# Optimization experiments

Measured on AMD Instinct MI355X. Metric: run time of the kernel, lower is better.

Reference implementation:

```python
import jax, jax.numpy as jnp
import numpy as np
import math

# ---- model dims (match init_kwargs) ----
D_MODEL = 1024
EXPAND = 2
HEADDIM = 64
D_STATE = 128
NGROUPS = 1
CHUNK = 64
A_FLOOR = 1e-4
D_INNER = EXPAND * D_MODEL            # 2048
NHEADS = D_INNER // HEADDIM           # 32
ROPE_DIM = D_STATE // 2               # rope_fraction=0.5 -> rotate half the state dims
NROPE = ROPE_DIM // 2                 # 32 rotation angles
D_IN_PROJ = D_INNER + 2 * D_STATE * NGROUPS + 3 * NHEADS + NROPE  # 2432
B, L = 2, 2048
EPS = 1e-5


def setup_inputs() -> dict:
    key = jax.random.key(0)
    ks = jax.random.split(key, 5)
    u = jax.random.normal(ks[0], (B, L, D_MODEL), dtype=jnp.float32)
    W_in = jax.random.normal(ks[1], (D_IN_PROJ, D_MODEL), dtype=jnp.float32) * 0.02
    W_out = jax.random.normal(ks[2], (D_MODEL, D_INNER), dtype=jnp.float32) * 0.02
    # dt_bias init as in the torch module
    dt_min, dt_max, dt_floor = 1e-3, 1e-1, 1e-4
    dt = jnp.exp(jax.random.uniform(ks[3], (NHEADS,)) * (math.log(dt_max) - math.log(dt_min)) + math.log(dt_min))
    dt = jnp.maximum(dt, dt_floor)
    dt_bias = dt + jnp.log(-jnp.expm1(-dt))
    B_bias = jnp.ones((NHEADS, D_STATE), dtype=jnp.float32)
    C_bias = jnp.ones((NHEADS, D_STATE), dtype=jnp.float32)
    Bnorm_w = jnp.ones((D_STATE,), dtype=jnp.float32)
    Cnorm_w = jnp.ones((D_STATE,), dtype=jnp.float32)
    D = jnp.ones((NHEADS,), dtype=jnp.float32)
    return {"u": u, "W_in": W_in, "dt_bias": dt_bias, "B_bias": B_bias, "C_bias": C_bias,
            "Bnorm_w": Bnorm_w, "Cnorm_w": Cnorm_w, "D": D, "W_out": W_out}


def _rmsnorm(v, w):
    return v * jax.lax.rsqrt(jnp.mean(v * v, axis=-1, keepdims=True) + EPS) * w


def _rope(v, cos, sin):
    # rotate first 2*NROPE dims of last axis (pairs (i, i+NROPE)); rest untouched
    x1 = v[..., :NROPE]
    x2 = v[..., NROPE:2 * NROPE]
    rest = v[..., 2 * NROPE:]
    return jnp.concatenate([x1 * cos - x2 * sin, x1 * sin + x2 * cos, rest], axis=-1)


def _forward(u, W_in, dt_bias, B_bias, C_bias, Bnorm_w, Cnorm_w, D, W_out):
    b, l, _ = u.shape
    proj = jnp.einsum('bld,ed->ble', u, W_in)
    idx = np.cumsum([D_INNER, D_STATE * NGROUPS, D_STATE * NGROUPS, NHEADS, NHEADS, NHEADS])[:-1].tolist()
    x, Braw, Craw, dd_dt, dd_A, trap_angles = jnp.split(proj, [D_INNER, D_INNER + D_STATE, D_INNER + 2 * D_STATE,
                                                                D_INNER + 2 * D_STATE + NHEADS,
                                                                D_INNER + 2 * D_STATE + 2 * NHEADS], axis=-1)
    trap = trap_angles[..., :NHEADS]
    angles = trap_angles[..., NHEADS:NHEADS + NROPE]
    x = x.reshape(b, l, NHEADS, HEADDIM)

    # discretization scalars per (b,l,h)
    A = -jax.nn.softplus(dd_A)
    A = jnp.minimum(A, -A_FLOOR)
    DT = jax.nn.softplus(dd_dt + dt_bias)
    la = A * DT                      # log of per-step decay (negative)
    a = jnp.exp(la)

    # RMSNorm on B/C (ngroups=1), broadcast to heads, add per-head bias
    Bn = _rmsnorm(Braw, Bnorm_w)[:, :, None, :] + B_bias   # (b,l,h,n)
    Cn = _rmsnorm(Craw, Cnorm_w)[:, :, None, :] + C_bias

    # inline RoPE: cumulative angle Theta_t = cumsum(angles_t * dt_t)
    theta = angles[:, :, None, :] * DT[..., None]           # (b,l,h,r)
    Theta = jnp.cumsum(theta, axis=1)
    cosT, sinT = jnp.cos(Theta), jnp.sin(Theta)
    Bn = _rope(Bn, cosT, sinT)
    Cn = _rope(Cn, cosT, sinT)

    # trapezoidal integration weights: dt*(lam*B_t x_t + (1-lam)*exp(A dt)*B_{t-1} x_{t-1})
    lam = jax.nn.sigmoid(trap)
    w1 = DT * lam                    # current-token weight  (b,l,h)
    w2 = DT * (1.0 - lam) * a        # previous-token weight (includes decay)
    Bp = jnp.pad(Bn, ((0, 0), (1, 0), (0, 0), (0, 0)))[:, :-1]
    xp = jnp.pad(x, ((0, 0), (1, 0), (0, 0), (0, 0)))[:, :-1]

    # ---- chunked selective scan ----
    nc = l // CHUNK
    ck = lambda t: t.reshape(b, nc, CHUNK, *t.shape[2:])
    xc, xpc, Bc, Bpc, Cc = ck(x), ck(xp), ck(Bn), ck(Bp), ck(Cn)
    lac, w1c, w2c = ck(la), ck(w1), ck(w2)
    Acum = jnp.cumsum(lac, axis=2)                           # (b,z,t,h)

    mask = jnp.tril(jnp.ones((CHUNK, CHUNK), dtype=u.dtype))
    decay = jnp.exp(Acum[:, :, :, None, :] - Acum[:, :, None, :, :]) * mask[None, None, :, :, None]  # (b,z,t,s,h)

    CB1 = jnp.einsum('bzthn,bzshn->bztsh', Cc, Bc)
    CB2 = jnp.einsum('bzthn,bzshn->bztsh', Cc, Bpc)
    M1 = decay * CB1 * w1c[:, :, None, :, :]
    M2 = decay * CB2 * w2c[:, :, None, :, :]
    Yintra = jnp.einsum('bztsh,bzshp->bzthp', M1, xc) + jnp.einsum('bztsh,bzshp->bzthp', M2, xpc)

    # contribution of each chunk to its end-of-chunk state
    r = jnp.exp(Acum[:, :, -1:, :] - Acum)                   # (b,z,t,h)
    U = (jnp.einsum('bzsh,bzshn,bzshp->bzhpn', r * w1c, Bc, xc)
         + jnp.einsum('bzsh,bzshn,bzshp->bzhpn', r * w2c, Bpc, xpc))
    cd = jnp.exp(Acum[:, :, -1, :])                          # whole-chunk decay (b,z,h)

    def step(h, inp):
        U_, c_ = inp
        return c_[..., None, None] * h + U_, h               # emit state at chunk start
    h0 = jnp.zeros((b, NHEADS, HEADDIM, D_STATE), dtype=u.dtype)
    _, states = jax.lax.scan(step, h0, (jnp.moveaxis(U, 1, 0), jnp.moveaxis(cd, 1, 0)))  # (z,b,h,p,n)

    Ystate = jnp.einsum('bzthn,bzth,zbhpn->bzthp', Cc, jnp.exp(Acum), states)
    y = (Yintra + Ystate).reshape(b, l, NHEADS, HEADDIM) + x * D[None, None, :, None]
    y = y.reshape(b, l, D_INNER)
    return jnp.einsum('bli,oi->blo', y, W_out)


def reference(u, W_in, dt_bias, B_bias, C_bias, Bnorm_w, Cnorm_w, D, W_out):
    return _forward(u, W_in, dt_bias, B_bias, C_bias, Bnorm_w, Cnorm_w, D, W_out)
```

## Files before the change

kernel.cpp:

```cpp
#include <hip/hip_runtime.h>
#include <hip/hip_bf16.h>
#include <math.h>

typedef unsigned short u16;
typedef __attribute__((ext_vector_type(8))) short s16x8;
typedef __attribute__((ext_vector_type(4))) float f32x4;

#define BB 2
#define LL 2048
#define DMODEL 1024
#define DI 2048
#define NH 32
#define HD 64
#define DS 128
#define NR 32
#define CH 64
#define NC 32
#define DIP 2432
#define NTOK (BB*LL)
#define PAW 384
#define CVW 264

__device__ __forceinline__ float bf2f(u16 u){ union{unsigned i; float f;} c; c.i=((unsigned)u)<<16; return c.f; }
__device__ __forceinline__ u16 f2bf(float f){ __hip_bfloat16 h=__float2bfloat16(f); return *reinterpret_cast<u16*>(&h); }
__device__ __forceinline__ float softplusf(float x){ return fmaxf(x,0.f) + log1pf(expf(-fabsf(x))); }

__device__ __forceinline__ void gl_lds16(const void* g, void* l){
  __builtin_amdgcn_global_load_lds((const __attribute__((address_space(1))) void*)g,
                                   (__attribute__((address_space(3))) void*)l, 16, 0, 0);
}

__device__ __forceinline__ s16x8 ldswz(const u16* base, int r, int kunit){
  return *(const s16x8*)&base[r*128 + ((kunit ^ (r&7))<<3)];
}
__device__ __forceinline__ s16x8 ldswz64(const u16* base, int r, int kunit){
  return *(const s16x8*)&base[r*64 + ((kunit ^ (r&7))<<3)];
}
__device__ __forceinline__ float ldswz64_s(const u16* base, int r, int n){
  return bf2f(base[r*64 + (((n>>3) ^ (r&7))<<3) + (n&7)]);
}
__device__ __forceinline__ s16x8 ld72(const u16* base, int r, int kelem){
  return *(const s16x8*)&base[r*72 + kelem];
}

__global__ __launch_bounds__(256) void k_cast(const float* __restrict__ in, u16* __restrict__ out, int n){
  int i = (blockIdx.x*256 + threadIdx.x)*4;
  if (i < n){
    float4 v = *(const float4*)&in[i];
    ushort4 o; o.x=f2bf(v.x); o.y=f2bf(v.y); o.z=f2bf(v.z); o.w=f2bf(v.w);
    *(ushort4*)&out[i] = o;
  }
}

__global__ __launch_bounds__(512) void k_gemm_in(const u16* __restrict__ A,
                                                 const u16* __restrict__ Bm,
                                                 float* __restrict__ pAux,
                                                 u16* __restrict__ Xtg){
  __shared__ u16 lA[128*64];
  __shared__ u16 lB[128*64];
  int tid = threadIdx.x;
  int l = tid & 63, w = tid >> 6;
  int nwg = gridDim.x*gridDim.y;
  int flat = blockIdx.y*gridDim.x + blockIdx.x;
  int cpx = nwg >> 3;
  int swz = (flat & 7)*cpx + (flat >> 3);
  int bx = swz % gridDim.x, by = swz / gridDim.x;
  int bm = by*128, bn = bx*128;
  int wr = w >> 2, wc = w & 3;
  const f32x4 vzero = {0.f,0.f,0.f,0.f};
  f32x4 acc[4][2];
  #pragma unroll
  for (int i=0;i<4;i++)
    #pragma unroll
    for (int j=0;j<2;j++) acc[i][j] = vzero;

  for (int kt=0; kt<DMODEL; kt+=64){
    __syncthreads();
    #pragma unroll
    for (int cc=0; cc<2; cc++){
      int s = w*2 + cc;
      int uu = s*64 + l;
      int r = uu >> 3, jl = uu & 7;
      int j = jl ^ (r & 7);
      gl_lds16(A  + (size_t)(bm+r)*DMODEL + kt + j*8, &lA[s*512]);
      gl_lds16(Bm + (size_t)(bn+r)*DMODEL + kt + j*8, &lB[s*512]);
    }
    __syncthreads();
    #pragma unroll
    for (int ks=0; ks<2; ks++){
      s16x8 af[4], bf[2];
      #pragma unroll
      for (int i=0;i<4;i++){
        int row = wr*64 + i*16 + (l&15);
        int j = ks*4 + (l>>4);
        af[i] = *(const s16x8*)&lA[row*64 + (j^(row&7))*8];
      }
      #pragma unroll
      for (int i=0;i<2;i++){
        int row = wc*32 + i*16 + (l&15);
        int j = ks*4 + (l>>4);
        bf[i] = *(const s16x8*)&lB[row*64 + (j^(row&7))*8];
      }
      #pragma unroll
      for (int i=0;i<4;i++)
        #pragma unroll
        for (int jj=0;jj<2;jj++)
          acc[i][jj] = __builtin_amdgcn_mfma_f32_16x16x32_bf16(af[i], bf[jj], acc[i][jj], 0,0,0);
    }
  }
  int col0 = bn + wc*32 + (l&15);
  int row0 = bm + wr*64 + (l>>4)*4;
  if (bn < DI){
    int h = (bn + wc*32) >> 6;
    int pbase = (wc & 1)*32 + (l&15);
    int b = bm >> 11;
    #pragma unroll
    for (int i=0;i<4;i++){
      int lbase = (bm & (LL-1)) + wr*64 + (l>>4)*4 + i*16;
      #pragma unroll
      for (int jj=0;jj<2;jj++){
        int p = pbase + jj*16;
        ushort4 o;
        o.x = f2bf(acc[i][jj][0]); o.y = f2bf(acc[i][jj][1]);
        o.z = f2bf(acc[i][jj][2]); o.w = f2bf(acc[i][jj][3]);
        *(ushort4*)&Xtg[((size_t)(b*NH + h)*HD + p)*LL + lbase] = o;
      }
    }
  } else {
    #pragma unroll
    for (int i=0;i<4;i++)
      #pragma unroll
      for (int jj=0;jj<2;jj++)
        #pragma unroll
        for (int q=0;q<4;q++)
          pAux[(size_t)(row0 + i*16 + q)*PAW + col0 + jj*16 - DI] = acc[i][jj][q];
  }
}

__global__ __launch_bounds__(256) void k_prep(const float* __restrict__ pAux,
                                              const float* __restrict__ dt_bias,
                                              const float* __restrict__ Bnw,
                                              const float* __restrict__ Cnw,
                                              float* __restrict__ Bnr, float* __restrict__ Cnr,
                                              float* __restrict__ DTg, float* __restrict__ lag,
                                              float* __restrict__ w1g, float* __restrict__ w2g){
  int tid = threadIdx.x;
  int r = tid >> 7, t = tid & 127;
  int row = blockIdx.x*2 + r;
  const float* pr = pAux + (size_t)row*PAW;
  float bv = pr[t], cv = pr[128+t];
  float sb = bv*bv, sc = cv*cv;
  for (int o=32;o;o>>=1){ sb += __shfl_down(sb,o); sc += __shfl_down(sc,o); }
  __shared__ float red[8];
  if ((tid&63)==0){ red[(tid>>6)*2]=sb; red[(tid>>6)*2+1]=sc; }
  __syncthreads();
  float ssb = red[r*4]+red[r*4+2], ssc = red[r*4+1]+red[r*4+3];
  float rb = rsqrtf(ssb/DS + 1e-5f), rc = rsqrtf(ssc/DS + 1e-5f);
  Bnr[(size_t)row*DS+t] = bv*rb*Bnw[t];
  Cnr[(size_t)row*DS+t] = cv*rc*Cnw[t];
  if (t < NH){
    int h = t;
    float Av = -softplusf(pr[288+h]); Av = fminf(Av, -1e-4f);
    float DT = softplusf(pr[256+h] + dt_bias[h]);
    float la = Av*DT;
    float lam = 1.f/(1.f+expf(-pr[320+h]));
    DTg[row*NH+h] = DT;
    lag[row*NH+h] = la;
    w1g[row*NH+h] = DT*lam;
    w2g[row*NH+h] = DT*(1.f-lam)*expf(la);
  }
}

__global__ __launch_bounds__(64) void k_theta_part(const float* __restrict__ pAux, const float* __restrict__ DTg,
                                                   float* __restrict__ Spart){
  int blk = blockIdx.x*2 + (threadIdx.x>>5);
  int j = threadIdx.x & 31;
  int h = blk % NH; int z = (blk/NH)%NC; int b = blk/(NH*NC);
  float acc = 0.f;
  for (int i=0;i<CH;i++){
    int row = b*LL + z*CH + i;
    acc += DTg[row*NH+h] * pAux[(size_t)row*PAW + 352 + j];
  }
  Spart[(size_t)blk*NR + j] = acc;
}

__global__ void k_theta_scan(float* __restrict__ Spart){
  int idx = blockIdx.x*blockDim.x + threadIdx.x;
  int j = idx % NR; int h = (idx/NR)%NH; int b = idx/(NR*NH);
  float acc = 0.f;
  for (int z=0;z<NC;z++){
    size_t o = (size_t)((b*NC+z)*NH + h)*NR + j;
    float t = Spart[o]; Spart[o] = acc; acc += t;
  }
}

__global__ __launch_bounds__(64) void k_theta_full(const float* __restrict__ pAux, const float* __restrict__ DTg,
                                                   const float* __restrict__ Spart, float* __restrict__ Theta){
  int blk = blockIdx.x*2 + (threadIdx.x>>5);
  int j = threadIdx.x & 31;
  int h = blk % NH; int z = (blk/NH)%NC; int b = blk/(NH*NC);
  float acc = Spart[(size_t)blk*NR + j];
  for (int i=0;i<CH;i++){
    int row = b*LL + z*CH + i;
    acc += DTg[row*NH+h] * pAux[(size_t)row*PAW + 352 + j];
    Theta[((size_t)row*NH + h)*NR + j] = acc;
  }
}

__global__ __launch_bounds__(256) void k_acum(const float* __restrict__ lag,
                                              const float* __restrict__ w1g,
                                              const float* __restrict__ w2g,
                                              float* __restrict__ CV,
                                              float* __restrict__ Acumg,
                                              float* __restrict__ cdg){
  int blk = blockIdx.x*4 + (threadIdx.x>>6);
  int l = threadIdx.x & 63;
  int h = blk & 31, z = (blk>>5)&31, b = blk>>10;
  int row = b*LL + z*CH + l;
  float la = lag[row*NH+h], w1 = w1g[row*NH+h], w2 = w2g[row*NH+h];
  float a = la;
  #pragma unroll
  for (int o=1;o<64;o<<=1){ float t = __shfl_up(a,o); a += (l>=o) ? t : 0.f; }
  float Acm = __shfl(a, 31);
  float Alast = __shfl(a, 63);
  float eA = expf(a - Acm);
  float emA = expf(Acm - a);
  float rfac = expf(Alast - a);
  float rw1 = rfac*w1, rw2 = rfac*w2;
  float rw1p = __shfl_up(rw1, 1);
  float* cv = CV + (size_t)blk*CVW;
  cv[l] = eA;
  cv[64 + l] = emA*w1;
  cv[128 + l] = emA*w2;
  cv[192 + l] = (l>0 ? rw1p : 0.f) + rw2;
  if (l == 63){ cv[192+64] = rw1; cdg[blk] = expf(Alast); }
  Acumg[(size_t)blk*CH + l] = a;
}

__global__ __launch_bounds__(256) void k_rope2(const float* __restrict__ Bnr,
                                               const float* __restrict__ Cnr,
                                               const float* __restrict__ Theta,
                                               const float* __restrict__ B_bias,
                                               const float* __restrict__ C_bias,
                                               const float* __restrict__ CV,
                                               u16* __restrict__ Bn, u16* __restrict__ Cn,
                                               u16* __restrict__ BTw){
  __shared__ float vwS[65];
  __shared__ u16 BTt[128][68];
  int blk = blockIdx.x; int h = blk&31, z=(blk>>5)&31, b=blk>>10;
  int l0 = z*CH; int tid = threadIdx.x;
  if (tid < 65) vwS[tid] = CV[(size_t)blk*CVW + 192 + tid];
  __syncthreads();
  #pragma unroll
  for (int it=0; it<8; it++){
    int idx = it*256 + tid;
    int r = idx>>5, j = idx&31;
    int row = b*LL + l0 + r;
    const float* br = Bnr + (size_t)row*DS;
    const float* cr = Cnr + (size_t)row*DS;
    const float* bb = B_bias + h*DS;
    const float* cb = C_bias + h*DS;
    float th = Theta[((size_t)row*NH + h)*NR + j];
    float cs = cosf(th), sn = sinf(th);
    float b0 = br[j]    + bb[j];
    float b1 = br[j+32] + bb[j+32];
    float b2 = br[j+64] + bb[j+64];
    float b3 = br[j+96] + bb[j+96];
    float c0 = cr[j]    + cb[j];
    float c1 = cr[j+32] + cb[j+32];
    float c2 = cr[j+64] + cb[j+64];
    float c3 = cr[j+96] + cb[j+96];
    float obA = b0*cs - b1*sn, obB = b0*sn + b1*cs;
    float ocA = c0*cs - c1*sn, ocB = c0*sn + c1*cs;
    u16* bnp = Bn + ((size_t)row*NH + h)*DS;
    u16* cnp = Cn + ((size_t)row*NH + h)*DS;
    bnp[j]    = f2bf(obA); bnp[j+32] = f2bf(obB);
    bnp[j+64] = f2bf(b2);  bnp[j+96] = f2bf(b3);
    cnp[j]    = f2bf(ocA); cnp[j+32] = f2bf(ocB);
    cnp[j+64] = f2bf(c2);  cnp[j+96] = f2bf(c3);
    float vwr = vwS[r+1];
    BTt[j][r]    = f2bf(obA*vwr);
    BTt[j+32][r] = f2bf(obB*vwr);
    BTt[j+64][r] = f2bf(b2*vwr);
    BTt[j+96][r] = f2bf(b3*vwr);
  }
  __syncthreads();
  for (int it=0; it<8; it++){
    int idx = it*256 + tid;
    int n = idx>>4, rg = (idx&15)*4;
    ushort4 o4 = *(ushort4*)&BTt[n][rg];
    *(ushort4*)&BTw[((size_t)((b*NH+h)*DS) + n)*LL + l0 + rg] = o4;
  }
}

__global__ __launch_bounds__(256) void k_chunk_a(
    const u16* __restrict__ Xtg, const u16* __restrict__ Bn,
    const u16* __restrict__ Cn, const u16* __restrict__ BTw,
    const float* __restrict__ CV, const float* __restrict__ Dgl,
    u16* __restrict__ Yb, u16* __restrict__ Ugb){
  __shared__ u16 BsBT[65*128];
  __shared__ u16 CsMc[64*128];
  __shared__ u16 Xt64[64*64];
  __shared__ u16 Bp[128], Xp[64];
  __shared__ float cvS[260];
  __shared__ float mc0s[64];
  int blk = blockIdx.x;
  int h = blk&31, z=(blk>>5)&31, b=blk>>10;
  int l0 = z*CH;
  int tid = threadIdx.x; int l = tid&63, w = tid>>6;
  size_t bh = (size_t)(b*NH + h);

  if (tid < 128){
    u16 v = 0;
    if (z > 0) v = Bn[((size_t)(b*LL+l0-1)*NH + h)*DS + tid];
    BsBT[tid] = v; Bp[tid] = v;
  } else if (tid < 192){
    int p = tid - 128;
    u16 v = 0;
    if (z > 0) v = Xtg[(bh*HD + p)*LL + l0 - 1];
    Xp[p] = v;
  }
  cvS[tid] = CV[(size_t)blk*CVW + tid];
  if (tid == 0) cvS[256] = CV[(size_t)blk*CVW + 256];
  #pragma unroll
  for (int cc=0; cc<4; cc++){
    int c = w*4 + cc;
    { int r = 1 + 4*c + (l>>4);
      gl_lds16(Bn + ((size_t)(b*LL+l0+r-1)*NH+h)*DS + (((l&15)^(r&7))<<3), &BsBT[(1+4*c)*128]); }
    { int r = 4*c + (l>>4);
      gl_lds16(Cn + ((size_t)(b*LL+l0+r)*NH+h)*DS + (((l&15)^(r&7))<<3), &CsMc[4*c*128]); }
  }
  #pragma unroll
  for (int cc=0; cc<2; cc++){
    int s = w*2 + cc;
    int uu = s*64 + l; int r = uu>>3, jl = uu&7, j = jl^(r&7);
    gl_lds16(Xtg + (bh*HD + r)*LL + l0 + j*8, &Xt64[s*512]);
  }
  __syncthreads();

  const f32x4 vzero = {0.f,0.f,0.f,0.f};
  f32x4 acb[4];
  #pragma unroll
  for (int j=0;j<4;j++) acb[j] = vzero;
  #pragma unroll
  for (int ks=0; ks<4; ks++){
    s16x8 af = ldswz(CsMc, 16*w + (l&15), ks*4 + (l>>4));
    #pragma unroll
    for (int j=0;j<4;j++){
      s16x8 bfr = ldswz(BsBT, 1 + 16*j + (l&15), ks*4 + (l>>4));
      acb[j] = __builtin_amdgcn_mfma_f32_16x16x32_bf16(af, bfr, acb[j], 0,0,0);
    }
  }
  {
    int t = tid>>2, part = tid&3;
    float s = 0.f;
    #pragma unroll
    for (int uu=0; uu<4; uu++){
      int u = part*4 + uu;
      s16x8 cr = *(const s16x8*)&CsMc[t*128 + ((u^(t&7))<<3)];
      s16x8 br = *(const s16x8*)&BsBT[u<<3];
      #pragma unroll
      for (int e=0;e<8;e++) s += bf2f(cr[e])*bf2f(br[e]);
    }
    s += __shfl_xor(s, 1); s += __shfl_xor(s, 2);
    if (part == 0) mc0s[t] = s * cvS[t] * cvS[128];
  }
  __syncthreads();

  #pragma unroll
  for (int cc=0; cc<4; cc++){
    int c = w*4 + cc;
    int uu = c*64 + l; int r = uu>>3, jl = uu&7, j = jl^(r&7);
    gl_lds16(BTw + (bh*DS + r)*LL + l0 + j*8, &BsBT[c*512]);
  }
  #pragma unroll
  for (int j=0;j<4;j++){
    #pragma unroll
    for (int q=0;q<4;q++){
      int t = 16*w + (l>>4)*4 + q;
      int k = 16*j + (l&15);
      int sp = k + 1;
      float g = 0.f;
      if (sp <= t+1) g += cvS[63+sp];
      if (sp <= t)   g += cvS[128+sp];
      g *= cvS[t];
      CsMc[t*72 + k] = f2bf(acb[j][q] * g);
    }
  }
  __syncthreads();

  f32x4 ay[4];
  #pragma unroll
  for (int j=0;j<4;j++) ay[j] = vzero;
  #pragma unroll
  for (int ks=0; ks<2; ks++){
    s16x8 af = ld72(CsMc, 16*w + (l&15), ks*32 + (l>>4)*8);
    #pragma unroll
    for (int j=0;j<4;j++){
      s16x8 bfr = ldswz64(Xt64, 16*j + (l&15), ks*4 + (l>>4));
      ay[j] = __builtin_amdgcn_mfma_f32_16x16x32_bf16(af, bfr, ay[j], 0,0,0);
    }
  }
  {
    float Dh = Dgl[h];
    #pragma unroll
    for (int j=0;j<4;j++){
      #pragma unroll
      for (int q=0;q<4;q++){
        int t = 16*w + (l>>4)*4 + q;
        int p = 16*j + (l&15);
        float xval = ldswz64_s(Xt64, p, t);
        float yv = ay[j][q] + mc0s[t]*bf2f(Xp[p]) + Dh*xval;
        Yb[((size_t)(b*LL + l0 + t))*DI + h*HD + p] = f2bf(yv);
      }
    }
  }

  f32x4 au[8];
  #pragma unroll
  for (int j=0;j<8;j++) au[j] = vzero;
  #pragma unroll
  for (int ks=0; ks<2; ks++){
    s16x8 af = ldswz64(Xt64, 16*w + (l&15), ks*4 + (l>>4));
    #pragma unroll
    for (int j=0;j<8;j++){
      s16x8 bfr = ldswz64(BsBT, 16*j + (l&15), ks*4 + (l>>4));
      au[j] = __builtin_amdgcn_mfma_f32_16x16x32_bf16(af, bfr, au[j], 0,0,0);
    }
  }
  {
    float vw0 = cvS[192];
    #pragma unroll
    for (int j=0;j<8;j++){
      #pragma unroll
      for (int q=0;q<4;q++){
        int p = 16*w + (l>>4)*4 + q;
        int n = 16*j + (l&15);
        float uv = au[j][q] + vw0*bf2f(Xp[p])*bf2f(Bp[n]);
        Ugb[(size_t)blk*(HD*DS) + p*DS + n] = f2bf(uv);
      }
    }
  }
}

__global__ __launch_bounds__(256) void k_scan(u16* __restrict__ Ugb, const float* __restrict__ cdg){
  int idx = blockIdx.x*256 + threadIdx.x;
  int pn = idx % (HD*DS);
  int h  = (idx/(HD*DS)) % NH;
  int b  = idx/(HD*DS*NH);
  float hs = 0.f;
  for (int z=0;z<NC;z++){
    size_t o = ((size_t)((b*NC+z)*NH) + h)*(HD*DS) + pn;
    float tmp = bf2f(Ugb[o]);
    Ugb[o] = f2bf(hs);
    hs = cdg[(b*NC+z)*NH + h]*hs + tmp;
  }
}

__global__ __launch_bounds__(256) void k_state(
    const u16* __restrict__ Cn, const u16* __restrict__ Ugb,
    const float* __restrict__ Acumg, u16* __restrict__ Yb){
  __shared__ u16 Cs[64*128];
  __shared__ u16 Sb[64*128];
  __shared__ float eAs[64];
  int blk = blockIdx.x;
  int h = blk & 31, z = (blk>>5)&31, b = blk>>10;
  int l0 = z*CH;
  int tid = threadIdx.x;
  int l = tid & 63, w = tid >> 6;

  if (tid < 64) eAs[tid] = expf(Acumg[(size_t)blk*CH + tid]);
  #pragma unroll
  for (int cc=0; cc<4; cc++){
    int c = w*4 + cc;
    int r = 4*c + (l>>4);
    gl_lds16(Cn + ((size_t)(b*LL + l0 + r)*NH + h)*DS + (((l&15)^(r&7))<<3), &Cs[4*c*128]);
    gl_lds16(Ugb + (size_t)blk*(HD*DS) + (size_t)r*DS + (((l&15)^(r&7))<<3), &Sb[4*c*128]);
  }
  __syncthreads();

  f32x4 as[4];
  const f32x4 vzero = {0.f,0.f,0.f,0.f};
  #pragma unroll
  for (int j=0;j<4;j++) as[j] = vzero;
  #pragma unroll
  for (int ks=0; ks<4; ks++){
    s16x8 af = ldswz(Cs, 16*w + (l&15), ks*4 + (l>>4));
    #pragma unroll
    for (int j=0;j<4;j++){
      s16x8 bfr = ldswz(Sb, 16*j + (l&15), ks*4 + (l>>4));
      as[j] = __builtin_amdgcn_mfma_f32_16x16x32_bf16(af, bfr, as[j], 0,0,0);
    }
  }
  #pragma unroll
  for (int j=0;j<4;j++){
    #pragma unroll
    for (int q=0;q<4;q++){
      int t = 16*w + (l>>4)*4 + q;
      int p = 16*j + (l&15);
      size_t idx = ((size_t)(b*LL + l0 + t))*DI + h*HD + p;
      Yb[idx] = f2bf(bf2f(Yb[idx]) + eAs[t]*as[j][q]);
    }
  }
}

template<int N, int K>
__global__ __launch_bounds__(512) void k_mfma_nt(const u16* __restrict__ A,
                                                 const u16* __restrict__ Bm,
                                                 float* __restrict__ C){
  __shared__ u16 lA[128*64];
  __shared__ u16 lB[128*64];
  int tid = threadIdx.x;
  int l = tid & 63, w = tid >> 6;
  int nwg = gridDim.x*gridDim.y;
  int flat = blockIdx.y*gridDim.x + blockIdx.x;
  int cpx = nwg >> 3;
  int swz = (flat & 7)*cpx + (flat >> 3);
  int bx = swz % gridDim.x, by = swz / gridDim.x;
  int bm = by*128, bn = bx*128;
  int wr = w >> 2, wc = w & 3;
  const f32x4 vzero = {0.f,0.f,0.f,0.f};
  f32x4 acc[4][2];
  #pragma unroll
  for (int i=0;i<4;i++)
    #pragma unroll
    for (int j=0;j<2;j++) acc[i][j] = vzero;

  for (int kt=0; kt<K; kt+=64){
    __syncthreads();
    #pragma unroll
    for (int cc=0; cc<2; cc++){
      int s = w*2 + cc;
      int uu = s*64 + l;
      int r = uu >> 3, jl = uu & 7;
      int j = jl ^ (r & 7);
      gl_lds16(A  + (size_t)(bm+r)*K + kt + j*8, &lA[s*512]);
      gl_lds16(Bm + (size_t)(bn+r)*K + kt + j*8, &lB[s*512]);
    }
    __syncthreads();
    #pragma unroll
    for (int ks=0; ks<2; ks++){
      s16x8 af[4], bf[2];
      #pragma unroll
      for (int i=0;i<4;i++){
        int row = wr*64 + i*16 + (l&15);
        int j = ks*4 + (l>>4);
        af[i] = *(const s16x8*)&lA[row*64 + (j^(row&7))*8];
      }
      #pragma unroll
      for (int i=0;i<2;i++){
        int row = wc*32 + i*16 + (l&15);
        int j = ks*4 + (l>>4);
        bf[i] = *(const s16x8*)&lB[row*64 + (j^(row&7))*8];
      }
      #pragma unroll
      for (int i=0;i<4;i++)
        #pragma unroll
        for (int jj=0;jj<2;jj++)
          acc[i][jj] = __builtin_amdgcn_mfma_f32_16x16x32_bf16(af[i], bf[jj], acc[i][jj], 0,0,0);
    }
  }
  int col0 = bn + wc*32 + (l&15);
  int row0 = bm + wr*64 + (l>>4)*4;
  #pragma unroll
  for (int i=0;i<4;i++)
    #pragma unroll
    for (int jj=0;jj<2;jj++)
      #pragma unroll
      for (int q=0;q<4;q++)
        C[(size_t)(row0 + i*16 + q)*N + col0 + jj*16] = acc[i][jj][q];
}

constexpr size_t OFF_PAUX  = 0;
constexpr size_t OFF_XTG   = 6291456;
constexpr size_t OFF_BNR   = 23068672;
constexpr size_t OFF_CNR   = 25165824;
constexpr size_t OFF_DT    = 27262976;
constexpr size_t OFF_LA    = 27787264;
constexpr size_t OFF_W1    = 28311552;
constexpr size_t OFF_W2    = 28835840;
constexpr size_t OFF_SPART = 29360128;
constexpr size_t OFF_CV    = 29622272;
constexpr size_t OFF_ACUM  = 31784960;
constexpr size_t OFF_CD    = 32309248;
constexpr size_t OFF_THETA = 32317440;
constexpr size_t OFF_Y     = OFF_THETA;
constexpr size_t OFF_BN    = 49094656;
constexpr size_t OFF_CN    = 82649088;
constexpr size_t OFF_BTW   = 116203520;
constexpr size_t OFF_R1    = 149757952;
constexpr size_t OFF_UBF   = OFF_R1;
constexpr size_t OFF_WINBF = OFF_R1 + 16777216;
constexpr size_t OFF_UGB   = OFF_R1;
constexpr size_t OFF_WOUTBF= OFF_PAUX;

extern "C" void kernel_launch(void* const* d_in, const int* in_sizes, int n_in,
                              void* d_out, int out_size, void* d_ws, size_t ws_size,
                              hipStream_t stream) {
  const float* u       = (const float*)d_in[0];
  const float* W_in    = (const float*)d_in[1];
  const float* dt_bias = (const float*)d_in[2];
  const float* B_bias  = (const float*)d_in[3];
  const float* C_bias  = (const float*)d_in[4];
  const float* Bnw     = (const float*)d_in[5];
  const float* Cnw     = (const float*)d_in[6];
  const float* Dg      = (const float*)d_in[7];
  const float* W_out   = (const float*)d_in[8];
  float* out = (float*)d_out;
  char* ws = (char*)d_ws;

  float* pAux  = (float*)(ws + OFF_PAUX);
  u16*   Xtg   = (u16*)  (ws + OFF_XTG);
  float* Bnr   = (float*)(ws + OFF_BNR);
  float* Cnr   = (float*)(ws + OFF_CNR);
  float* DTg   = (float*)(ws + OFF_DT);
  float* lag   = (float*)(ws + OFF_LA);
  float* w1g   = (float*)(ws + OFF_W1);
  float* w2g   = (float*)(ws + OFF_W2);
  float* Spart = (float*)(ws + OFF_SPART);
  float* CVp   = (float*)(ws + OFF_CV);
  float* Acumg = (float*)(ws + OFF_ACUM);
  float* cdg   = (float*)(ws + OFF_CD);
  float* Theta = (float*)(ws + OFF_THETA);
  u16*   Yb    = (u16*)  (ws + OFF_Y);
  u16*   Bn    = (u16*)  (ws + OFF_BN);
  u16*   Cn    = (u16*)  (ws + OFF_CN);
  u16*   BTw   = (u16*)  (ws + OFF_BTW);
  u16*   u_bf  = (u16*)  (ws + OFF_UBF);
  u16*   Win_bf= (u16*)  (ws + OFF_WINBF);
  u16*   Ugb   = (u16*)  (ws + OFF_UGB);
  u16*   Wout_bf=(u16*)  (ws + OFF_WOUTBF);

  k_cast<<<(NTOK*DMODEL)/1024, 256, 0, stream>>>(u, u_bf, NTOK*DMODEL);
  k_cast<<<(DIP*DMODEL)/1024, 256, 0, stream>>>(W_in, Win_bf, DIP*DMODEL);
  k_gemm_in<<<dim3(DIP/128, NTOK/128), 512, 0, stream>>>(u_bf, Win_bf, pAux, Xtg);

  k_prep      <<<NTOK/2, 256, 0, stream>>>(pAux, dt_bias, Bnw, Cnw, Bnr, Cnr, DTg, lag, w1g, w2g);
  k_theta_part<<<(BB*NC*NH)/2, 64, 0, stream>>>(pAux, DTg, Spart);
  k_theta_scan<<<(BB*NH*NR)/256, 256, 0, stream>>>(Spart);
  k_theta_full<<<(BB*NC*NH)/2, 64, 0, stream>>>(pAux, DTg, Spart, Theta);
  k_acum      <<<(BB*NC*NH)/4, 256, 0, stream>>>(lag, w1g, w2g, CVp, Acumg, cdg);
  k_rope2     <<<BB*NC*NH, 256, 0, stream>>>(Bnr, Cnr, Theta, B_bias, C_bias, CVp, Bn, Cn, BTw);

  k_chunk_a<<<BB*NC*NH, 256, 0, stream>>>(Xtg, Bn, Cn, BTw, CVp, Dg, Yb, Ugb);
  k_scan   <<<(BB*NH*HD*DS)/256, 256, 0, stream>>>(Ugb, cdg);
  k_state  <<<BB*NC*NH, 256, 0, stream>>>(Cn, Ugb, Acumg, Yb);

  k_cast<<<(DMODEL*DI)/1024, 256, 0, stream>>>(W_out, Wout_bf, DMODEL*DI);
  k_mfma_nt<DMODEL, DI><<<dim3(DMODEL/128, NTOK/128), 512, 0, stream>>>(Yb, Wout_bf, out);

  (void)in_sizes; (void)n_in; (void)out_size; (void)ws_size;
}
```

Baseline: 189.7 us.

## Fuse B rope into chunk kernel and vectorize the inter-chunk scan

B-side RoPE, bias add and the weighted transposed copy are now computed inside k_chunk_a directly into shared memory, instead of being written to global Bn/BTw buffers and reloaded. This removes two large per-head bf16 intermediates and their global round trips. The Y buffer moves to a separate workspace offset, since it can no longer alias Theta, which k_chunk_a now reads. k_scan now handles 8 state elements per thread with 16-byte loads and stores, using fewer threads. The cost is extra trig and LDS work in the chunk kernel, plus less parallelism in the scan.

```diff
diff --git a/kernel.cpp b/kernel.cpp
--- a/kernel.cpp
+++ b/kernel.cpp
@@ -32,6 +32,9 @@
 
 __device__ __forceinline__ s16x8 ldswz(const u16* base, int r, int kunit){
   return *(const s16x8*)&base[r*128 + ((kunit ^ (r&7))<<3)];
+}
+__device__ __forceinline__ int swze(int row, int n){
+  return row*128 + ((((n>>3) ^ (row&7))<<3) | (n&7));
 }
 __device__ __forceinline__ s16x8 ldswz64(const u16* base, int r, int kunit){
   return *(const s16x8*)&base[r*64 + ((kunit ^ (r&7))<<3)];
@@ -237,69 +240,41 @@
   Acumg[(size_t)blk*CH + l] = a;
 }
 
-__global__ __launch_bounds__(256) void k_rope2(const float* __restrict__ Bnr,
-                                               const float* __restrict__ Cnr,
+__global__ __launch_bounds__(256) void k_ropeC(const float* __restrict__ Cnr,
                                                const float* __restrict__ Theta,
-                                               const float* __restrict__ B_bias,
                                                const float* __restrict__ C_bias,
-                                               const float* __restrict__ CV,
-                                               u16* __restrict__ Bn, u16* __restrict__ Cn,
-                                               u16* __restrict__ BTw){
-  __shared__ float vwS[65];
-  __shared__ u16 BTt[128][68];
+                                               u16* __restrict__ Cn){
   int blk = blockIdx.x; int h = blk&31, z=(blk>>5)&31, b=blk>>10;
   int l0 = z*CH; int tid = threadIdx.x;
-  if (tid < 65) vwS[tid] = CV[(size_t)blk*CVW + 192 + tid];
-  __syncthreads();
+  const float* cb = C_bias + h*DS;
   #pragma unroll
   for (int it=0; it<8; it++){
     int idx = it*256 + tid;
     int r = idx>>5, j = idx&31;
     int row = b*LL + l0 + r;
-    const float* br = Bnr + (size_t)row*DS;
     const float* cr = Cnr + (size_t)row*DS;
-    const float* bb = B_bias + h*DS;
-    const float* cb = C_bias + h*DS;
     float th = Theta[((size_t)row*NH + h)*NR + j];
     float cs = cosf(th), sn = sinf(th);
-    float b0 = br[j]    + bb[j];
-    float b1 = br[j+32] + bb[j+32];
-    float b2 = br[j+64] + bb[j+64];
-    float b3 = br[j+96] + bb[j+96];
     float c0 = cr[j]    + cb[j];
     float c1 = cr[j+32] + cb[j+32];
     float c2 = cr[j+64] + cb[j+64];
     float c3 = cr[j+96] + cb[j+96];
-    float obA = b0*cs - b1*sn, obB = b0*sn + b1*cs;
     float ocA = c0*cs - c1*sn, ocB = c0*sn + c1*cs;
-    u16* bnp = Bn + ((size_t)row*NH + h)*DS;
     u16* cnp = Cn + ((size_t)row*NH + h)*DS;
-    bnp[j]    = f2bf(obA); bnp[j+32] = f2bf(obB);
-    bnp[j+64] = f2bf(b2);  bnp[j+96] = f2bf(b3);
     cnp[j]    = f2bf(ocA); cnp[j+32] = f2bf(ocB);
     cnp[j+64] = f2bf(c2);  cnp[j+96] = f2bf(c3);
-    float vwr = vwS[r+1];
-    BTt[j][r]    = f2bf(obA*vwr);
-    BTt[j+32][r] = f2bf(obB*vwr);
-    BTt[j+64][r] = f2bf(b2*vwr);
-    BTt[j+96][r] = f2bf(b3*vwr);
-  }
-  __syncthreads();
-  for (int it=0; it<8; it++){
-    int idx = it*256 + tid;
-    int n = idx>>4, rg = (idx&15)*4;
-    ushort4 o4 = *(ushort4*)&BTt[n][rg];
-    *(ushort4*)&BTw[((size_t)((b*NH+h)*DS) + n)*LL + l0 + rg] = o4;
   }
 }
 
 __global__ __launch_bounds__(256) void k_chunk_a(
-    const u16* __restrict__ Xtg, const u16* __restrict__ Bn,
-    const u16* __restrict__ Cn, const u16* __restrict__ BTw,
+    const u16* __restrict__ Xtg, const float* __restrict__ Bnr,
+    const u16* __restrict__ Cn, const float* __restrict__ Theta,
+    const float* __restrict__ B_bias,
     const float* __restrict__ CV, const float* __restrict__ Dgl,
     u16* __restrict__ Yb, u16* __restrict__ Ugb){
-  __shared__ u16 BsBT[65*128];
+  __shared__ u16 Bs[65*128];
   __shared__ u16 CsMc[64*128];
+  __shared__ u16 Bt[128*72];
   __shared__ u16 Xt64[64*64];
   __shared__ u16 Bp[128], Xp[64];
   __shared__ float cvS[260];
@@ -310,25 +285,19 @@
   int tid = threadIdx.x; int l = tid&63, w = tid>>6;
   size_t bh = (size_t)(b*NH + h);
 
-  if (tid < 128){
-    u16 v = 0;
-    if (z > 0) v = Bn[((size_t)(b*LL+l0-1)*NH + h)*DS + tid];
-    BsBT[tid] = v; Bp[tid] = v;
-  } else if (tid < 192){
+  cvS[tid] = CV[(size_t)blk*CVW + tid];
+  if (tid == 0) cvS[256] = CV[(size_t)blk*CVW + 256];
+  if (tid >= 128 && tid < 192){
     int p = tid - 128;
     u16 v = 0;
     if (z > 0) v = Xtg[(bh*HD + p)*LL + l0 - 1];
     Xp[p] = v;
   }
-  cvS[tid] = CV[(size_t)blk*CVW + tid];
-  if (tid == 0) cvS[256] = CV[(size_t)blk*CVW + 256];
   #pragma unroll
   for (int cc=0; cc<4; cc++){
     int c = w*4 + cc;
-    { int r = 1 + 4*c + (l>>4);
-      gl_lds16(Bn + ((size_t)(b*LL+l0+r-1)*NH+h)*DS + (((l&15)^(r&7))<<3), &BsBT[(1+4*c)*128]); }
-    { int r = 4*c + (l>>4);
-      gl_lds16(Cn + ((size_t)(b*LL+l0+r)*NH+h)*DS + (((l&15)^(r&7))<<3), &CsMc[4*c*128]); }
+    int r = 4*c + (l>>4);
+    gl_lds16(Cn + ((size_t)(b*LL+l0+r)*NH+h)*DS + (((l&15)^(r&7))<<3), &CsMc[4*c*128]);
   }
   #pragma unroll
   for (int cc=0; cc<2; cc++){
@@ -338,6 +307,54 @@
   }
   __syncthreads();
 
+  {
+    const float* bb = B_bias + h*DS;
+    #pragma unroll
+    for (int it=0; it<8; it++){
+      int idx = it*256 + tid;
+      int r = idx>>5, j = idx&31;
+      int row = b*LL + l0 + r;
+      const float* br = Bnr + (size_t)row*DS;
+      float th = Theta[((size_t)row*NH + h)*NR + j];
+      float cs = cosf(th), sn = sinf(th);
+      float b0 = br[j]    + bb[j];
+      float b1 = br[j+32] + bb[j+32];
+      float b2 = br[j+64] + bb[j+64];
+      float b3 = br[j+96] + bb[j+96];
+      float obA = b0*cs - b1*sn, obB = b0*sn + b1*cs;
+      int rr = r + 1;
+      Bs[swze(rr, j)]    = f2bf(obA);
+      Bs[swze(rr, j+32)] = f2bf(obB);
+      Bs[swze(rr, j+64)] = f2bf(b2);
+      Bs[swze(rr, j+96)] = f2bf(b3);
+      float vwr = cvS[192 + rr];
+      Bt[j*72 + r]      = f2bf(obA*vwr);
+      Bt[(j+32)*72 + r] = f2bf(obB*vwr);
+      Bt[(j+64)*72 + r] = f2bf(b2*vwr);
+      Bt[(j+96)*72 + r] = f2bf(b3*vwr);
+    }
+    if (tid < 32){
+      int j = tid;
+      float obA=0.f, obB=0.f, b2=0.f, b3=0.f;
+      if (z > 0){
+        int row = b*LL + l0 - 1;
+        const float* br = Bnr + (size_t)row*DS;
+        float th = Theta[((size_t)row*NH + h)*NR + j];
+        float cs = cosf(th), sn = sinf(th);
+        float b0 = br[j]    + bb[j];
+        float b1 = br[j+32] + bb[j+32];
+        b2 = br[j+64] + bb[j+64];
+        b3 = br[j+96] + bb[j+96];
+        obA = b0*cs - b1*sn; obB = b0*sn + b1*cs;
+      }
+      Bs[j]    = f2bf(obA); Bs[j+32] = f2bf(obB);
+      Bs[j+64] = f2bf(b2);  Bs[j+96] = f2bf(b3);
+      Bp[j]    = f2bf(obA); Bp[j+32] = f2bf(obB);
+      Bp[j+64] = f2bf(b2);  Bp[j+96] = f2bf(b3);
+    }
+  }
+  __syncthreads();
+
   const f32x4 vzero = {0.f,0.f,0.f,0.f};
   f32x4 acb[4];
   #pragma unroll
@@ -347,7 +364,7 @@
     s16x8 af = ldswz(CsMc, 16*w + (l&15), ks*4 + (l>>4));
     #pragma unroll
     for (int j=0;j<4;j++){
-      s16x8 bfr = ldswz(BsBT, 1 + 16*j + (l&15), ks*4 + (l>>4));
+      s16x8 bfr = ldswz(Bs, 1 + 16*j + (l&15), ks*4 + (l>>4));
       acb[j] = __builtin_amdgcn_mfma_f32_16x16x32_bf16(af, bfr, acb[j], 0,0,0);
     }
   }
@@ -358,7 +375,7 @@
     for (int uu=0; uu<4; uu++){
       int u = part*4 + uu;
       s16x8 cr = *(const s16x8*)&CsMc[t*128 + ((u^(t&7))<<3)];
-      s16x8 br = *(const s16x8*)&BsBT[u<<3];
+      s16x8 br = *(const s16x8*)&Bs[u<<3];
       #pragma unroll
       for (int e=0;e<8;e++) s += bf2f(cr[e])*bf2f(br[e]);
     }
@@ -367,12 +384,6 @@
   }
   __syncthreads();
 
-  #pragma unroll
-  for (int cc=0; cc<4; cc++){
-    int c = w*4 + cc;
-    int uu = c*64 + l; int r = uu>>3, jl = uu&7, j = jl^(r&7);
-    gl_lds16(BTw + (bh*DS + r)*LL + l0 + j*8, &BsBT[c*512]);
-  }
   #pragma unroll
   for (int j=0;j<4;j++){
     #pragma unroll
@@ -424,7 +435,7 @@
     s16x8 af = ldswz64(Xt64, 16*w + (l&15), ks*4 + (l>>4));
     #pragma unroll
     for (int j=0;j<8;j++){
-      s16x8 bfr = ldswz64(BsBT, 16*j + (l&15), ks*4 + (l>>4));
+      s16x8 bfr = ld72(Bt, 16*j + (l&15), ks*32 + (l>>4)*8);
       au[j] = __builtin_amdgcn_mfma_f32_16x16x32_bf16(af, bfr, au[j], 0,0,0);
     }
   }
@@ -445,15 +456,24 @@
 
 __global__ __launch_bounds__(256) void k_scan(u16* __restrict__ Ugb, const float* __restrict__ cdg){
   int idx = blockIdx.x*256 + threadIdx.x;
-  int pn = idx % (HD*DS);
-  int h  = (idx/(HD*DS)) % NH;
-  int b  = idx/(HD*DS*NH);
-  float hs = 0.f;
+  int pn8 = (idx & 1023)*8;
+  int h  = (idx >> 10) & 31;
+  int b  = idx >> 15;
+  float hs[8];
+  #pragma unroll
+  for (int e=0;e<8;e++) hs[e] = 0.f;
   for (int z=0;z<NC;z++){
-    size_t o = ((size_t)((b*NC+z)*NH) + h)*(HD*DS) + pn;
-    float tmp = bf2f(Ugb[o]);
-    Ugb[o] = f2bf(hs);
-    hs = cdg[(b*NC+z)*NH + h]*hs + tmp;
+    size_t o = ((size_t)((b*NC+z)*NH) + h)*(HD*DS) + pn8;
+    s16x8 v = *(s16x8*)&Ugb[o];
+    float cd = cdg[(b*NC+z)*NH + h];
+    s16x8 wv;
+    #pragma unroll
+    for (int e=0;e<8;e++){
+      float tmp = bf2f((u16)v[e]);
+      wv[e] = (short)f2bf(hs[e]);
+      hs[e] = cd*hs[e] + tmp;
+    }
+    *(s16x8*)&Ugb[o] = wv;
   }
 }
 
@@ -584,10 +604,8 @@
 constexpr size_t OFF_ACUM  = 31784960;
 constexpr size_t OFF_CD    = 32309248;
 constexpr size_t OFF_THETA = 32317440;
-constexpr size_t OFF_Y     = OFF_THETA;
-constexpr size_t OFF_BN    = 49094656;
+constexpr size_t OFF_Y     = 49094656;
 constexpr size_t OFF_CN    = 82649088;
-constexpr size_t OFF_BTW   = 116203520;
 constexpr size_t OFF_R1    = 149757952;
 constexpr size_t OFF_UBF   = OFF_R1;
 constexpr size_t OFF_WINBF = OFF_R1 + 16777216;
@@ -623,9 +641,7 @@
   float* cdg   = (float*)(ws + OFF_CD);
   float* Theta = (float*)(ws + OFF_THETA);
   u16*   Yb    = (u16*)  (ws + OFF_Y);
-  u16*   Bn    = (u16*)  (ws + OFF_BN);
   u16*   Cn    = (u16*)  (ws + OFF_CN);
-  u16*   BTw   = (u16*)  (ws + OFF_BTW);
   u16*   u_bf  = (u16*)  (ws + OFF_UBF);
   u16*   Win_bf= (u16*)  (ws + OFF_WINBF);
   u16*   Ugb   = (u16*)  (ws + OFF_UGB);
@@ -640,10 +656,10 @@
   k_theta_scan<<<(BB*NH*NR)/256, 256, 0, stream>>>(Spart);
   k_theta_full<<<(BB*NC*NH)/2, 64, 0, stream>>>(pAux, DTg, Spart, Theta);
   k_acum      <<<(BB*NC*NH)/4, 256, 0, stream>>>(lag, w1g, w2g, CVp, Acumg, cdg);
-  k_rope2     <<<BB*NC*NH, 256, 0, stream>>>(Bnr, Cnr, Theta, B_bias, C_bias, CVp, Bn, Cn, BTw);
-
-  k_chunk_a<<<BB*NC*NH, 256, 0, stream>>>(Xtg, Bn, Cn, BTw, CVp, Dg, Yb, Ugb);
-  k_scan   <<<(BB*NH*HD*DS)/256, 256, 0, stream>>>(Ugb, cdg);
+  k_ropeC     <<<BB*NC*NH, 256, 0, stream>>>(Cnr, Theta, C_bias, Cn);
+
+  k_chunk_a<<<BB*NC*NH, 256, 0, stream>>>(Xtg, Bnr, Cn, Theta, B_bias, CVp, Dg, Yb, Ugb);
+  k_scan   <<<(BB*NH*HD*DS)/(256*8), 256, 0, stream>>>(Ugb, cdg);
   k_state  <<<BB*NC*NH, 256, 0, stream>>>(Cn, Ugb, Acumg, Yb);
 
   k_cast<<<(DMODEL*DI)/1024, 256, 0, stream>>>(W_out, Wout_bf, DMODEL*DI);
```

After: 195.3 us. 1.03x slower.
